# Performance work log

Measured on AMD Instinct MI355X. Metric: run time of the kernel, lower is better.

## Reference

```python
import jax, jax.numpy as jnp
import numpy as np

N = 100000   # nodes
E = 800000   # edges
D = 64       # hidden_channels
H = 4        # heads
C = D        # out_channels per head (PyG: out_channels=hidden)


def setup_inputs() -> dict:
    key = jax.random.key(0)
    ks = jax.random.split(key, 20)
    inp = {}
    inp['x'] = jax.random.normal(ks[0], (N, D), dtype=jnp.float32)
    inp['edge_index'] = jax.random.randint(ks[1], (2, E), 0, N, dtype=jnp.int32)
    i = 2
    for layer in (1, 2):
        for nm in ('Wq', 'Wk', 'Wv'):
            inp[f'{nm}{layer}'] = jax.random.normal(ks[i], (D, H * C), dtype=jnp.float32) * 0.05; i += 1
            inp[f'b{nm[1]}{layer}'] = jnp.zeros((H * C,), dtype=jnp.float32)
        inp[f'Ws{layer}'] = jax.random.normal(ks[i], (D, D), dtype=jnp.float32) * 0.05; i += 1
        inp[f'bs{layer}'] = jnp.zeros((D,), dtype=jnp.float32)
    return inp


def _transformer_conv(x, src, dst, Wq, bq, Wk, bk, Wv, bv, Ws, bs):
    n = x.shape[0]
    q = (x @ Wq + bq).reshape(n, H, C)
    k = (x @ Wk + bk).reshape(n, H, C)
    v = (x @ Wv + bv).reshape(n, H, C)
    # per-edge attention logits: [E, H]
    alpha = jnp.einsum('ehc,ehc->eh', q[dst], k[src]) / np.sqrt(C).astype(np.float32)
    # segment softmax over incoming edges of each destination node
    amax = jax.ops.segment_max(alpha, dst, num_segments=n)          # [N, H]
    ex = jnp.exp(alpha - amax[dst])                                 # [E, H]
    denom = jax.ops.segment_sum(ex, dst, num_segments=n)           # [N, H]
    attn = ex / (denom[dst] + 1e-16)                                # [E, H]
    msg = v[src] * attn[:, :, None]                                 # [E, H, C]
    agg = jax.ops.segment_sum(msg, dst, num_segments=n)            # [N, H, C]
    # concat=False -> mean over heads; root_weight skip connection
    return agg.mean(axis=1) + x @ Ws + bs


def reference(x, edge_index, Wq1, bq1, Wk1, bk1, Wv1, bv1, Ws1, bs1,
              Wq2, bq2, Wk2, bk2, Wv2, bv2, Ws2, bs2):
    src, dst = edge_index[0], edge_index[1]
    h = _transformer_conv(x, src, dst, Wq1, bq1, Wk1, bk1, Wv1, bv1, Ws1, bs1)
    h = jax.nn.relu(h)
    out = _transformer_conv(h, src, dst, Wq2, bq2, Wk2, bk2, Wv2, bv2, Ws2, bs2)
    return out
```

## Files before the change

### kernel.cpp

```cpp
#include <hip/hip_runtime.h>
#include <hip/hip_fp16.h>
#include <math.h>


typedef __attribute__((ext_vector_type(8))) short bf16x8;
typedef __attribute__((ext_vector_type(4))) float f32x4;
typedef __attribute__((ext_vector_type(2))) float f32x2;

#define QKSCALE 32.0f
#define C_EXP2 1.760325e-4f

__device__ inline unsigned short f2bf(float f) {
    unsigned int u = __float_as_uint(f);
    u = (u + 0x7fffu + ((u >> 16) & 1u)) >> 16;
    return (unsigned short)u;
}

#if __has_builtin(__builtin_amdgcn_cvt_pk_fp8_f32) && __has_builtin(__builtin_amdgcn_cvt_pk_f32_fp8)
#define HW_FP8 1
#endif

#ifndef HW_FP8
__device__ inline unsigned int fp8_enc1(float f) {
    unsigned int u = __float_as_uint(f);
    unsigned int s = (u >> 24) & 0x80u;
    float a = fabsf(f);
    if (a >= 448.f) return s | 0x7Eu;
    if (a < 0.015625f) return s;
    unsigned int ua = __float_as_uint(a);
    unsigned int r = ua + 0x7FFFFu + ((ua >> 20) & 1u);
    int e = (int)((r >> 23) & 255u) - 120;
    unsigned int m = (r >> 20) & 7u;
    if (e < 1) return s;
    if (e > 15) return s | 0x7Eu;
    return s | (unsigned int)((e << 3) | m);
}
__device__ inline float fp8_dec1(unsigned int b) {
    unsigned int e = (b >> 3) & 15u, m = b & 7u;
    float v;
    if (e) v = __uint_as_float(((e + 120u) << 23) | (m << 20));
    else   v = (float)m * 0.001953125f;
    return (b & 0x80u) ? -v : v;
}
#endif

__device__ inline unsigned int fp8x4_pack(float f0, float f1, float f2, float f3) {
#ifdef HW_FP8
    int pk = __builtin_amdgcn_cvt_pk_fp8_f32(f0, f1, 0, false);
    pk = __builtin_amdgcn_cvt_pk_fp8_f32(f2, f3, pk, true);
    return (unsigned int)pk;
#else
    return fp8_enc1(f0) | (fp8_enc1(f1) << 8) | (fp8_enc1(f2) << 16) | (fp8_enc1(f3) << 24);
#endif
}

__device__ inline float4 fp8x4_unpack(unsigned int k) {
#ifdef HW_FP8
    f32x2 lo = __builtin_amdgcn_cvt_pk_f32_fp8((int)k, false);
    f32x2 hi = __builtin_amdgcn_cvt_pk_f32_fp8((int)k, true);
    return make_float4(lo[0], lo[1], hi[0], hi[1]);
#else
    return make_float4(fp8_dec1(k & 255u), fp8_dec1((k >> 8) & 255u),
                       fp8_dec1((k >> 16) & 255u), fp8_dec1(k >> 24));
#endif
}

__device__ inline unsigned int i8x4_pack(float f0, float f1, float f2, float f3) {
    int a = (int)rintf(f0 * QKSCALE); a = a < -127 ? -127 : (a > 127 ? 127 : a);
    int b = (int)rintf(f1 * QKSCALE); b = b < -127 ? -127 : (b > 127 ? 127 : b);
    int c = (int)rintf(f2 * QKSCALE); c = c < -127 ? -127 : (c > 127 ? 127 : c);
    int d = (int)rintf(f3 * QKSCALE); d = d < -127 ? -127 : (d > 127 ? 127 : d);
    return (unsigned int)((a & 255) | ((b & 255) << 8) | ((c & 255) << 16) | ((d & 255) << 24));
}

__device__ inline int sdot4(unsigned int a, unsigned int b, int c) {
#if __has_builtin(__builtin_amdgcn_sdot4)
    return __builtin_amdgcn_sdot4((int)a, (int)b, c, false);
#else
    int r = c;
#pragma unroll
    for (int i = 0; i < 4; ++i) {
        int ai = (int)(a << (24 - 8 * i)) >> 24;
        int bi = (int)(b << (24 - 8 * i)) >> 24;
        r += ai * bi;
    }
    return r;
#endif
}

__global__ void k_setup(
    const float* __restrict__ x, unsigned short* __restrict__ Xb, int ncast4,
    const float* __restrict__ Wq1, const float* __restrict__ Wk1,
    const float* __restrict__ Wv1, const float* __restrict__ Ws1,
    const float* __restrict__ Wq2, const float* __restrict__ Wk2,
    const float* __restrict__ Wv2, const float* __restrict__ Ws2,
    unsigned short* __restrict__ Wt,
    int* __restrict__ counts, int N, int castBl)
{
    int b = blockIdx.x, tid = threadIdx.x;
    if (b < castBl) {
        int i = b * 256 + tid;
        if (i < ncast4) {
            float4 v = ((const float4*)x)[i];
            ushort4 o;
            o.x = f2bf(v.x); o.y = f2bf(v.y); o.z = f2bf(v.z); o.w = f2bf(v.w);
            ((ushort4*)Xb)[i] = o;
        }
    } else if (b < castBl + 416) {
        int j = (b - castBl) * 256 + tid;
        int layer = j / 53248;
        int r = j % 53248;
        if (r < 49152) {
            int m = r / 16384, w = r % 16384;
            int n = w / 64, k = w % 64;
            const float* W = (layer == 0)
                ? ((m == 0) ? Wq1 : (m == 1) ? Wk1 : Wv1)
                : ((m == 0) ? Wq2 : (m == 1) ? Wk2 : Wv2);
            Wt[layer * 53248 + m * 16384 + n * 64 + k] = f2bf(W[k * 256 + n]);
        } else {
            int w = r - 49152;
            int n = w / 64, k = w % 64;
            const float* W = (layer == 0) ? Ws1 : Ws2;
            Wt[layer * 53248 + 49152 + n * 64 + k] = f2bf(W[k * 64 + n]);
        }
    } else {
        int i = (b - castBl - 416) * 256 + tid;
        if (i < N) counts[i] = 0;
    }
}

#define SCAN_B 256
#define SCAN_CHUNK 2048
__global__ void k_scan1(const int* __restrict__ counts, int n,
                        int* __restrict__ offs, int* __restrict__ bsums) {
    __shared__ int lds[SCAN_B];
    int b = blockIdx.x, tid = threadIdx.x;
    int base = b * SCAN_CHUNK + tid * 8;
    int v[8]; int s = 0;
#pragma unroll
    for (int i = 0; i < 8; ++i) { int idx = base + i; int c = (idx < n) ? counts[idx] : 0; v[i] = s; s += c; }
    lds[tid] = s;
    for (int off = 1; off < SCAN_B; off <<= 1) {
        __syncthreads();
        int x = (tid >= off) ? lds[tid - off] : 0;
        __syncthreads();
        lds[tid] += x;
    }
    __syncthreads();
    int texcl = lds[tid] - s;
#pragma unroll
    for (int i = 0; i < 8; ++i) { int idx = base + i; if (idx < n) offs[idx] = texcl + v[i]; }
    if (tid == SCAN_B - 1) bsums[b] = lds[tid];
}

__global__ void k_scan2(int* bsums, int nb) {
    __shared__ int lds[256];
    int t = threadIdx.x;
    if (nb > 256) {
        if (t == 0) { int s = 0; for (int i = 0; i < nb; ++i) { int c = bsums[i]; bsums[i] = s; s += c; } }
        return;
    }
    int v = (t < nb) ? bsums[t] : 0;
    lds[t] = v;
    for (int off = 1; off < 256; off <<= 1) {
        __syncthreads();
        int x = (t >= off) ? lds[t - off] : 0;
        __syncthreads();
        lds[t] += x;
    }
    __syncthreads();
    if (t < nb) bsums[t] = lds[t] - v;
}

__global__ void k_scatter(const int* __restrict__ src, const int* __restrict__ dst, int E,
                          const int* __restrict__ offs, const int* __restrict__ bsums,
                          const int* __restrict__ rank, int* __restrict__ csr_src) {
    int e = blockIdx.x * 256 + threadIdx.x;
    if (e < E) {
        int d = dst[e];
        csr_src[offs[d] + bsums[d >> 11] + rank[e]] = src[e];
    }
}

#define GST 68
__global__ __launch_bounds__(256, 2) void k_gemm(
    const unsigned short* __restrict__ Xb, int nrows,
    const unsigned short* __restrict__ WtL,
    const float* __restrict__ bqp, const float* __restrict__ bkp,
    const float* __restrict__ bvp, const float* __restrict__ bsp,
    unsigned char* __restrict__ NB,
    const int* __restrict__ dstp, int histE,
    int* __restrict__ counts, int* __restrict__ rank, int gemmBl, int ntiles)
{
    __shared__ unsigned char st[4][64 * GST];
    __shared__ float bias[832];
    int tid = threadIdx.x;
    if (blockIdx.x >= gemmBl) {
        int e = (blockIdx.x - gemmBl) * 256 + tid;
        if (e < histE) rank[e] = atomicAdd(&counts[dstp[e]], 1);
        return;
    }
    int qtr = tid >> 6, lane = tid & 63;
    int quad = lane >> 4, n16 = lane & 15;
    unsigned char* wst = st[qtr];

    if (tid < 208) {
        float4 b4;
        if (tid < 64)       b4 = ((const float4*)bqp)[tid];
        else if (tid < 128) b4 = ((const float4*)bkp)[tid - 64];
        else if (tid < 192) b4 = ((const float4*)bvp)[tid - 128];
        else                b4 = ((const float4*)bsp)[tid - 192];
        ((float4*)bias)[tid] = b4;
    }

    const unsigned short* Wq = WtL;
    const unsigned short* Wk = WtL + 16384;
    const unsigned short* Wv = WtL + 32768;
    const unsigned short* Ws = WtL + 49152;
    bf16x8 fQ[8], fK[8], fV[8], fS[2];
#pragma unroll
    for (int c = 0; c < 4; ++c) {
        int roff = ((qtr * 4 + c) * 16 + n16) * 64 + quad * 8;
        fQ[2 * c]     = *(const bf16x8*)(Wq + roff);
        fQ[2 * c + 1] = *(const bf16x8*)(Wq + roff + 32);
        fK[2 * c]     = *(const bf16x8*)(Wk + roff);
        fK[2 * c + 1] = *(const bf16x8*)(Wk + roff + 32);
        fV[2 * c]     = *(const bf16x8*)(Wv + roff);
        fV[2 * c + 1] = *(const bf16x8*)(Wv + roff + 32);
    }
    {
        int roff = (qtr * 16 + n16) * 64 + quad * 8;
        fS[0] = *(const bf16x8*)(Ws + roff);
        fS[1] = *(const bf16x8*)(Ws + roff + 32);
    }
    __syncthreads();

    auto loadA = [&](int t, bf16x8 (&x0)[4], bf16x8 (&x1)[4]) {
        int r0 = t * 64;
#pragma unroll
        for (int g = 0; g < 4; ++g) {
            int node = r0 + g * 16 + n16;
            int nodec = (node < nrows) ? node : (nrows - 1);
            x0[g] = *(const bf16x8*)(Xb + (size_t)nodec * 64 + quad * 8);
            x1[g] = *(const bf16x8*)(Xb + (size_t)nodec * 64 + 32 + quad * 8);
        }
    };

    auto do_mat = [&](const bf16x8 (&fm)[8], int boff, int matoff, bool isInt8,
                      int r0, const bf16x8 (&x0)[4], const bf16x8 (&x1)[4]) {
#pragma unroll
        for (int c = 0; c < 4; ++c) {
            float4 cb = *(const float4*)(bias + boff + qtr * 64 + c * 16 + quad * 4);
#pragma unroll
            for (int g = 0; g < 4; ++g) {
                f32x4 acc = {cb.x, cb.y, cb.z, cb.w};
                acc = __builtin_amdgcn_mfma_f32_16x16x32_bf16(fm[2 * c],     x0[g], acc, 0, 0, 0);
                acc = __builtin_amdgcn_mfma_f32_16x16x32_bf16(fm[2 * c + 1], x1[g], acc, 0, 0, 0);
                unsigned int pk = isInt8 ? i8x4_pack(acc[0], acc[1], acc[2], acc[3])
                                         : fp8x4_pack(acc[0], acc[1], acc[2], acc[3]);
                *(unsigned int*)(wst + (g * 16 + n16) * GST + c * 16 + quad * 4) = pk;
            }
        }
#pragma unroll
        for (int it = 0; it < 4; ++it) {
            int row = it * 16 + (lane >> 2);
            uint4 v = *(const uint4*)(wst + row * GST + (lane & 3) * 16);
            int nd = r0 + row;
            if (nd < nrows)
                *(uint4*)(NB + (size_t)nd * 1024 + matoff + qtr * 64 + (lane & 3) * 16) = v;
        }
    };

    bf16x8 a0[4], a1[4], b0[4], b1[4];
    int t = blockIdx.x;
    if (t < ntiles) loadA(t, a0, a1);
    for (; t < ntiles; t += gemmBl) {
        int tn = t + gemmBl;
        if (tn < ntiles) loadA(tn, b0, b1);
        int r0 = t * 64;
        do_mat(fQ, 0,   0,   true,  r0, a0, a1);
        do_mat(fK, 256, 256, true,  r0, a0, a1);
        do_mat(fV, 512, 512, false, r0, a0, a1);
        {
            float4 cs = *(const float4*)(bias + 768 + qtr * 16 + quad * 4);
#pragma unroll
            for (int g = 0; g < 4; ++g) {
                f32x4 acc = {cs.x, cs.y, cs.z, cs.w};
                acc = __builtin_amdgcn_mfma_f32_16x16x32_bf16(fS[0], a0[g], acc, 0, 0, 0);
                acc = __builtin_amdgcn_mfma_f32_16x16x32_bf16(fS[1], a1[g], acc, 0, 0, 0);
                *(float4*)(wst + (g * 16 + n16) * GST + quad * 16) =
                    make_float4(acc[0], acc[1], acc[2], acc[3]);
            }
#pragma unroll
            for (int it = 0; it < 4; ++it) {
                int row = it * 16 + (lane >> 2);
                uint4 v = *(const uint4*)(wst + row * GST + (lane & 3) * 16);
                int nd = r0 + row;
                if (nd < nrows)
                    *(uint4*)(NB + (size_t)nd * 1024 + 768 + qtr * 64 + (lane & 3) * 16) = v;
            }
        }
#pragma unroll
        for (int g = 0; g < 4; ++g) { a0[g] = b0[g]; a1[g] = b1[g]; }
    }
}

__global__ __launch_bounds__(256) void k_attn(
    const unsigned char* __restrict__ NB,
    const int* __restrict__ offs, const int* __restrict__ bsums,
    const int* __restrict__ csr_src,
    float* __restrict__ out, unsigned short* __restrict__ Xb,
    int n, int Etot, int mode)
{
    int node = blockIdx.x * 4 + (threadIdx.x >> 6);
    if (node >= n) return;
    int lane = threadIdx.x & 63;
    int sl = lane & 31;
    int half = lane >> 5;
    uint2 q8 = *(const uint2*)(NB + (size_t)node * 1024 + sl * 8);
    int beg = offs[node] + bsums[node >> 11];
    int end = (node + 1 < n) ? (offs[node + 1] + bsums[(node + 1) >> 11]) : Etot;
    float l = 0.f;
    float acc[8];
#pragma unroll
    for (int i = 0; i < 8; ++i) acc[i] = 0.f;
    for (int base = beg; base < end; base += 8) {
        int cnt = end - base; if (cnt > 8) cnt = 8;
        int my = (lane < cnt) ? csr_src[base + lane] : 0;
        uint2 kk[4], vv[4];
#pragma unroll
        for (int p = 0; p < 4; ++p) {
            int idx = __shfl(my, 2 * p + half);
            const unsigned char* row = NB + (size_t)idx * 1024 + 256 + sl * 8;
            kk[p] = *(const uint2*)(row);
            vv[p] = *(const uint2*)(row + 256);
        }
#pragma unroll
        for (int p = 0; p < 4; ++p) {
            int d = sdot4(kk[p].x, q8.x, 0);
            d = sdot4(kk[p].y, q8.y, d);
            d += __shfl_xor(d, 1); d += __shfl_xor(d, 2); d += __shfl_xor(d, 4);
            float w = __builtin_exp2f((float)d * C_EXP2);
            w = (2 * p + half < cnt) ? w : 0.f;
            l += w;
            float4 va = fp8x4_unpack(vv[p].x);
            float4 vb = fp8x4_unpack(vv[p].y);
            acc[0] += va.x * w; acc[1] += va.y * w;
            acc[2] += va.z * w; acc[3] += va.w * w;
            acc[4] += vb.x * w; acc[5] += vb.y * w;
            acc[6] += vb.z * w; acc[7] += vb.w * w;
        }
    }
    l += __shfl_xor(l, 32);
#pragma unroll
    for (int i = 0; i < 8; ++i) acc[i] += __shfl_xor(acc[i], 32);
    float inv = 1.f / (l + 1e-16f);
#pragma unroll
    for (int i = 0; i < 8; ++i) acc[i] *= inv;
#pragma unroll
    for (int i = 0; i < 8; ++i) {
        acc[i] += __shfl_xor(acc[i], 8);
        acc[i] += __shfl_xor(acc[i], 16);
        acc[i] *= 0.25f;
    }
    if (lane < 8) {
        const float* Srow = (const float*)(NB + (size_t)node * 1024 + 768);
        float4 s0 = *(const float4*)(Srow + lane * 8);
        float4 s1 = *(const float4*)(Srow + lane * 8 + 4);
        float r0 = acc[0] + s0.x, r1 = acc[1] + s0.y;
        float r2 = acc[2] + s0.z, r3 = acc[3] + s0.w;
        float r4 = acc[4] + s1.x, r5 = acc[5] + s1.y;
        float r6 = acc[6] + s1.z, r7 = acc[7] + s1.w;
        if (mode == 1) {
            r0 = fmaxf(r0, 0.f); r1 = fmaxf(r1, 0.f);
            r2 = fmaxf(r2, 0.f); r3 = fmaxf(r3, 0.f);
            r4 = fmaxf(r4, 0.f); r5 = fmaxf(r5, 0.f);
            r6 = fmaxf(r6, 0.f); r7 = fmaxf(r7, 0.f);
            uint4 o;
            o.x = (unsigned int)f2bf(r0) | ((unsigned int)f2bf(r1) << 16);
            o.y = (unsigned int)f2bf(r2) | ((unsigned int)f2bf(r3) << 16);
            o.z = (unsigned int)f2bf(r4) | ((unsigned int)f2bf(r5) << 16);
            o.w = (unsigned int)f2bf(r6) | ((unsigned int)f2bf(r7) << 16);
            *(uint4*)(Xb + (size_t)node * 64 + lane * 8) = o;
        } else {
            *(float4*)(out + (size_t)node * 64 + lane * 8) = make_float4(r0, r1, r2, r3);
            *(float4*)(out + (size_t)node * 64 + lane * 8 + 4) = make_float4(r4, r5, r6, r7);
        }
    }
}

extern "C" void kernel_launch(void* const* d_in, const int* in_sizes, int n_in,
                              void* d_out, int out_size, void* d_ws, size_t ws_size,
                              hipStream_t stream)
{
    const float* x  = (const float*)d_in[0];
    const int*   ei = (const int*)d_in[1];
    int N = in_sizes[0] / 64;
    int E = in_sizes[1] / 2;
    const int* srcp = ei;
    const int* dstp = ei + E;
    const float* Wq1 = (const float*)d_in[2],  *bq1 = (const float*)d_in[3];
    const float* Wk1 = (const float*)d_in[4],  *bk1 = (const float*)d_in[5];
    const float* Wv1 = (const float*)d_in[6],  *bv1 = (const float*)d_in[7];
    const float* Ws1 = (const float*)d_in[8],  *bs1 = (const float*)d_in[9];
    const float* Wq2 = (const float*)d_in[10], *bq2 = (const float*)d_in[11];
    const float* Wk2 = (const float*)d_in[12], *bk2 = (const float*)d_in[13];
    const float* Wv2 = (const float*)d_in[14], *bv2 = (const float*)d_in[15];
    const float* Ws2 = (const float*)d_in[16], *bs2 = (const float*)d_in[17];
    float* out = (float*)d_out;

    char* ws = (char*)d_ws;
    size_t off = 0;
    auto alloc = [&](size_t bytes) -> void* {
        void* p = ws + off;
        off = (off + bytes + 255) & ~(size_t)255;
        return p;
    };
    unsigned short* Xb = (unsigned short*)alloc((size_t)N * 64 * 2);
    unsigned char* NB  = (unsigned char*)alloc(((size_t)N + 64) * 1024);
    unsigned short* Wt = (unsigned short*)alloc(2 * 53248 * 2);
    int* counts = (int*)alloc((size_t)N * 4);
    int* rank   = (int*)alloc((size_t)E * 4);
    int* offs   = (int*)alloc((size_t)N * 4);
    int* bsums  = (int*)alloc(1024 * 4);
    int* csr    = (int*)alloc((size_t)E * 4);
    (void)n_in; (void)out_size;
    if (off > ws_size) return;

    int ebl = (E + 255) / 256;
    int nb_scan = (N + SCAN_CHUNK - 1) / SCAN_CHUNK;
    int ntiles = (N + 63) / 64;
    int gemm_bl = ntiles < 512 ? ntiles : 512;
    int hist_bl = (E + 255) / 256;
    int attn_bl = (N + 3) / 4;
    int ncast4 = N * 16;
    int castBl = (ncast4 + 255) / 256;
    int zeroBl = (N + 255) / 256;

    k_setup<<<castBl + 416 + zeroBl, 256, 0, stream>>>(
        x, Xb, ncast4, Wq1, Wk1, Wv1, Ws1, Wq2, Wk2, Wv2, Ws2, Wt, counts, N, castBl);

    k_gemm<<<gemm_bl + hist_bl, 256, 0, stream>>>(
        Xb, N, Wt, bq1, bk1, bv1, bs1, NB,
        dstp, E, counts, rank, gemm_bl, ntiles);

    k_scan1<<<nb_scan, SCAN_B, 0, stream>>>(counts, N, offs, bsums);
    k_scan2<<<1, 256, 0, stream>>>(bsums, nb_scan);
    k_scatter<<<ebl, 256, 0, stream>>>(srcp, dstp, E, offs, bsums, rank, csr);

    k_attn<<<attn_bl, 256, 0, stream>>>(NB, offs, bsums, csr, out, Xb, N, E, 1);

    k_gemm<<<gemm_bl, 256, 0, stream>>>(
        Xb, N, Wt + 53248, bq2, bk2, bv2, bs2, NB,
        dstp, 0, counts, rank, gemm_bl, ntiles);

    k_attn<<<attn_bl, 256, 0, stream>>>(NB, offs, bsums, csr, out, Xb, N, E, 0);
}
```

Baseline: 366.6 us.

## Split node buffer into separate Q/K/V/S planes and prefetch CSR indices

Replaces the interleaved 1 KB-per-node record with four separate 256-byte-per-node planes for Q, K, V and the skip term. The attention kernel's random K and V gathers then touch dense, separate arrays. The kernel also prefetches the next batch of CSR source indices one iteration ahead, and accumulates V with packed two-wide FMAs using 32-bit offset arithmetic. The costs are more live registers and two separate gather streams per edge instead of one contiguous 512-byte region.

```diff
diff --git a/kernel.cpp b/kernel.cpp
--- a/kernel.cpp
+++ b/kernel.cpp
@@ -51,17 +51,6 @@
     return (unsigned int)pk;
 #else
     return fp8_enc1(f0) | (fp8_enc1(f1) << 8) | (fp8_enc1(f2) << 16) | (fp8_enc1(f3) << 24);
-#endif
-}
-
-__device__ inline float4 fp8x4_unpack(unsigned int k) {
-#ifdef HW_FP8
-    f32x2 lo = __builtin_amdgcn_cvt_pk_f32_fp8((int)k, false);
-    f32x2 hi = __builtin_amdgcn_cvt_pk_f32_fp8((int)k, true);
-    return make_float4(lo[0], lo[1], hi[0], hi[1]);
-#else
-    return make_float4(fp8_dec1(k & 255u), fp8_dec1((k >> 8) & 255u),
-                       fp8_dec1((k >> 16) & 255u), fp8_dec1(k >> 24));
 #endif
 }
 
@@ -188,7 +177,8 @@
     const unsigned short* __restrict__ WtL,
     const float* __restrict__ bqp, const float* __restrict__ bkp,
     const float* __restrict__ bvp, const float* __restrict__ bsp,
-    unsigned char* __restrict__ NB,
+    unsigned char* __restrict__ Qp, unsigned char* __restrict__ Kp,
+    unsigned char* __restrict__ Vp, unsigned char* __restrict__ Sp,
     const int* __restrict__ dstp, int histE,
     int* __restrict__ counts, int* __restrict__ rank, int gemmBl, int ntiles)
 {
@@ -246,8 +236,9 @@
         }
     };
 
-    auto do_mat = [&](const bf16x8 (&fm)[8], int boff, int matoff, bool isInt8,
-                      int r0, const bf16x8 (&x0)[4], const bf16x8 (&x1)[4]) {
+    auto do_mat = [&](const bf16x8 (&fm)[8], int boff, unsigned char* plane,
+                      bool isInt8, int r0,
+                      const bf16x8 (&x0)[4], const bf16x8 (&x1)[4]) {
 #pragma unroll
         for (int c = 0; c < 4; ++c) {
             float4 cb = *(const float4*)(bias + boff + qtr * 64 + c * 16 + quad * 4);
@@ -267,7 +258,7 @@
             uint4 v = *(const uint4*)(wst + row * GST + (lane & 3) * 16);
             int nd = r0 + row;
             if (nd < nrows)
-                *(uint4*)(NB + (size_t)nd * 1024 + matoff + qtr * 64 + (lane & 3) * 16) = v;
+                *(uint4*)(plane + (size_t)nd * 256 + qtr * 64 + (lane & 3) * 16) = v;
         }
     };
 
@@ -278,9 +269,9 @@
         int tn = t + gemmBl;
         if (tn < ntiles) loadA(tn, b0, b1);
         int r0 = t * 64;
-        do_mat(fQ, 0,   0,   true,  r0, a0, a1);
-        do_mat(fK, 256, 256, true,  r0, a0, a1);
-        do_mat(fV, 512, 512, false, r0, a0, a1);
+        do_mat(fQ, 0,   Qp, true,  r0, a0, a1);
+        do_mat(fK, 256, Kp, true,  r0, a0, a1);
+        do_mat(fV, 512, Vp, false, r0, a0, a1);
         {
             float4 cs = *(const float4*)(bias + 768 + qtr * 16 + quad * 4);
 #pragma unroll
@@ -297,7 +288,7 @@
                 uint4 v = *(const uint4*)(wst + row * GST + (lane & 3) * 16);
                 int nd = r0 + row;
                 if (nd < nrows)
-                    *(uint4*)(NB + (size_t)nd * 1024 + 768 + qtr * 64 + (lane & 3) * 16) = v;
+                    *(uint4*)(Sp + (size_t)nd * 256 + qtr * 64 + (lane & 3) * 16) = v;
             }
         }
 #pragma unroll
@@ -306,7 +297,8 @@
 }
 
 __global__ __launch_bounds__(256) void k_attn(
-    const unsigned char* __restrict__ NB,
+    const unsigned char* __restrict__ Qp, const unsigned char* __restrict__ Kp,
+    const unsigned char* __restrict__ Vp, const float* __restrict__ Sp,
     const int* __restrict__ offs, const int* __restrict__ bsums,
     const int* __restrict__ csr_src,
     float* __restrict__ out, unsigned short* __restrict__ Xb,
@@ -317,23 +309,25 @@
     int lane = threadIdx.x & 63;
     int sl = lane & 31;
     int half = lane >> 5;
-    uint2 q8 = *(const uint2*)(NB + (size_t)node * 1024 + sl * 8);
+    unsigned slb = (unsigned)sl * 8u;
+    uint2 q8 = *(const uint2*)(Qp + ((unsigned)node << 8) + slb);
     int beg = offs[node] + bsums[node >> 11];
     int end = (node + 1 < n) ? (offs[node + 1] + bsums[(node + 1) >> 11]) : Etot;
     float l = 0.f;
-    float acc[8];
-#pragma unroll
-    for (int i = 0; i < 8; ++i) acc[i] = 0.f;
+    f32x2 acc2[4];
+#pragma unroll
+    for (int i = 0; i < 4; ++i) acc2[i] = (f32x2){0.f, 0.f};
+    int my = (beg + lane < end) ? csr_src[beg + lane] : 0;
     for (int base = beg; base < end; base += 8) {
+        int myn = (base + 8 + lane < end) ? csr_src[base + 8 + lane] : 0;
         int cnt = end - base; if (cnt > 8) cnt = 8;
-        int my = (lane < cnt) ? csr_src[base + lane] : 0;
         uint2 kk[4], vv[4];
 #pragma unroll
         for (int p = 0; p < 4; ++p) {
             int idx = __shfl(my, 2 * p + half);
-            const unsigned char* row = NB + (size_t)idx * 1024 + 256 + sl * 8;
-            kk[p] = *(const uint2*)(row);
-            vv[p] = *(const uint2*)(row + 256);
+            unsigned off = ((unsigned)idx << 8) + slb;
+            kk[p] = *(const uint2*)(Kp + off);
+            vv[p] = *(const uint2*)(Vp + off);
         }
 #pragma unroll
         for (int p = 0; p < 4; ++p) {
@@ -343,14 +337,27 @@
             float w = __builtin_exp2f((float)d * C_EXP2);
             w = (2 * p + half < cnt) ? w : 0.f;
             l += w;
-            float4 va = fp8x4_unpack(vv[p].x);
-            float4 vb = fp8x4_unpack(vv[p].y);
-            acc[0] += va.x * w; acc[1] += va.y * w;
-            acc[2] += va.z * w; acc[3] += va.w * w;
-            acc[4] += vb.x * w; acc[5] += vb.y * w;
-            acc[6] += vb.z * w; acc[7] += vb.w * w;
-        }
-    }
+            f32x2 w2 = {w, w};
+#ifdef HW_FP8
+            f32x2 va = __builtin_amdgcn_cvt_pk_f32_fp8((int)vv[p].x, false);
+            f32x2 vb = __builtin_amdgcn_cvt_pk_f32_fp8((int)vv[p].x, true);
+            f32x2 vc = __builtin_amdgcn_cvt_pk_f32_fp8((int)vv[p].y, false);
+            f32x2 vd = __builtin_amdgcn_cvt_pk_f32_fp8((int)vv[p].y, true);
+#else
+            f32x2 va = {fp8_dec1(vv[p].x & 255u), fp8_dec1((vv[p].x >> 8) & 255u)};
+            f32x2 vb = {fp8_dec1((vv[p].x >> 16) & 255u), fp8_dec1(vv[p].x >> 24)};
+            f32x2 vc = {fp8_dec1(vv[p].y & 255u), fp8_dec1((vv[p].y >> 8) & 255u)};
+            f32x2 vd = {fp8_dec1((vv[p].y >> 16) & 255u), fp8_dec1(vv[p].y >> 24)};
+#endif
+            acc2[0] = __builtin_elementwise_fma(va, w2, acc2[0]);
+            acc2[1] = __builtin_elementwise_fma(vb, w2, acc2[1]);
+            acc2[2] = __builtin_elementwise_fma(vc, w2, acc2[2]);
+            acc2[3] = __builtin_elementwise_fma(vd, w2, acc2[3]);
+        }
+        my = myn;
+    }
+    float acc[8] = {acc2[0][0], acc2[0][1], acc2[1][0], acc2[1][1],
+                    acc2[2][0], acc2[2][1], acc2[3][0], acc2[3][1]};
     l += __shfl_xor(l, 32);
 #pragma unroll
     for (int i = 0; i < 8; ++i) acc[i] += __shfl_xor(acc[i], 32);
@@ -364,7 +371,7 @@
         acc[i] *= 0.25f;
     }
     if (lane < 8) {
-        const float* Srow = (const float*)(NB + (size_t)node * 1024 + 768);
+        const float* Srow = Sp + ((size_t)node << 6);
         float4 s0 = *(const float4*)(Srow + lane * 8);
         float4 s1 = *(const float4*)(Srow + lane * 8 + 4);
         float r0 = acc[0] + s0.x, r1 = acc[1] + s0.y;
@@ -417,7 +424,10 @@
         return p;
     };
     unsigned short* Xb = (unsigned short*)alloc((size_t)N * 64 * 2);
-    unsigned char* NB  = (unsigned char*)alloc(((size_t)N + 64) * 1024);
+    unsigned char* Qp  = (unsigned char*)alloc(((size_t)N + 64) * 256);
+    unsigned char* Kp  = (unsigned char*)alloc(((size_t)N + 64) * 256);
+    unsigned char* Vp  = (unsigned char*)alloc(((size_t)N + 64) * 256);
+    unsigned char* Sp  = (unsigned char*)alloc(((size_t)N + 64) * 256);
     unsigned short* Wt = (unsigned short*)alloc(2 * 53248 * 2);
     int* counts = (int*)alloc((size_t)N * 4);
     int* rank   = (int*)alloc((size_t)E * 4);
@@ -441,18 +451,20 @@
         x, Xb, ncast4, Wq1, Wk1, Wv1, Ws1, Wq2, Wk2, Wv2, Ws2, Wt, counts, N, castBl);
 
     k_gemm<<<gemm_bl + hist_bl, 256, 0, stream>>>(
-        Xb, N, Wt, bq1, bk1, bv1, bs1, NB,
+        Xb, N, Wt, bq1, bk1, bv1, bs1, Qp, Kp, Vp, Sp,
         dstp, E, counts, rank, gemm_bl, ntiles);
 
     k_scan1<<<nb_scan, SCAN_B, 0, stream>>>(counts, N, offs, bsums);
     k_scan2<<<1, 256, 0, stream>>>(bsums, nb_scan);
     k_scatter<<<ebl, 256, 0, stream>>>(srcp, dstp, E, offs, bsums, rank, csr);
 
-    k_attn<<<attn_bl, 256, 0, stream>>>(NB, offs, bsums, csr, out, Xb, N, E, 1);
+    k_attn<<<attn_bl, 256, 0, stream>>>(Qp, Kp, Vp, (const float*)Sp,
+                                        offs, bsums, csr, out, Xb, N, E, 1);
 
     k_gemm<<<gemm_bl, 256, 0, stream>>>(
-        Xb, N, Wt + 53248, bq2, bk2, bv2, bs2, NB,
+        Xb, N, Wt + 53248, bq2, bk2, bv2, bs2, Qp, Kp, Vp, Sp,
         dstp, 0, counts, rank, gemm_bl, ntiles);
 
-    k_attn<<<attn_bl, 256, 0, stream>>>(NB, offs, bsums, csr, out, Xb, N, E, 0);
-}
+    k_attn<<<attn_bl, 256, 0, stream>>>(Qp, Kp, Vp, (const float*)Sp,
+                                        offs, bsums, csr, out, Xb, N, E, 0);
+}
```

Measured after the change: 362.3 us. Within noise of the previous version (-1.2%).
